# Optimization experiments

Measured on AMD Instinct MI355X. Metric: run time of the kernel, lower is better.

## Reference

```python
import jax, jax.numpy as jnp
import numpy as np
import math

E, N, K, R = 1024, 16, 4, 64  # embed_dim, state_dim, d_conv, dt_rank=ceil(E/16)
B, L = 2, 2048


def setup_inputs() -> dict:
    key = jax.random.key(0)
    ks = jax.random.split(key, 8)
    gn = lambda k, sh, sc: jax.random.normal(k, sh, dtype=jnp.float32) * sc
    W_z = gn(ks[0], (E, E), E ** -0.5)                      # in_proj_z weight (no bias)
    W_params = gn(ks[1], (R + 2 * N, E), E ** -0.5)         # in_proj_params weight (no bias)
    conv_w = gn(ks[2], (E, 1, K), 0.5)                      # depthwise conv1d weight, no bias
    dt_std = R ** -0.5 * 0.1
    W_dt = jax.random.uniform(ks[3], (E, R), jnp.float32, -dt_std, dt_std)
    b_dt = jnp.full((E,), math.log(math.expm1(0.001)), dtype=jnp.float32)
    A_log = jnp.tile(jnp.log(jnp.arange(1, N + 1, dtype=jnp.float32))[None, :], (E, 1))
    D = jnp.ones((E,), dtype=jnp.float32)
    W_out = gn(ks[4], (E, E), E ** -0.5)
    x = jax.random.normal(ks[5], (B, L, E), dtype=jnp.float32)
    return dict(x=x, W_z=W_z, W_params=W_params, conv_w=conv_w, W_dt=W_dt,
                b_dt=b_dt, A_log=A_log, D=D, W_out=W_out)


def reference(x, W_z, W_params, conv_w, W_dt, b_dt, A_log, D, W_out):
    b, l, e = x.shape
    n = A_log.shape[1]
    r = W_dt.shape[1]
    k = conv_w.shape[-1]

    z = x @ W_z.T                                           # [B,L,E]
    params = x @ W_params.T                                 # [B,L,R+2N]
    dt_unproj = params[..., :r]
    # B_proj = params[..., r:r+n] is computed but UNUSED in the original forward
    C_proj = params[..., r + n:]                            # [B,L,N]
    dt = jax.nn.softplus(dt_unproj @ W_dt.T + b_dt)         # [B,L,E]

    # depthwise causal conv: torch pads K-1 both sides then slices [:L] == left-pad K-1
    xc = jax.lax.conv_general_dilated(
        x.transpose(0, 2, 1), conv_w, (1,), [(k - 1, 0)],
        dimension_numbers=('NCH', 'OIH', 'NCH'), feature_group_count=e)
    u = jax.nn.silu(xc.transpose(0, 2, 1))                  # [B,L,E]

    A = -jnp.exp(A_log)                                     # [E,N]
    A_tilde = jnp.exp(dt[..., None] * A[None, None])        # [B,L,E,N]
    B_tilde = jnp.where(jnp.abs(A)[None, None] < 1e-5,
                        dt[..., None],
                        (A_tilde - 1.0) / (A[None, None] + 1e-10))

    # recurrence (note t-1 indexing, faithful to original):
    # h_0 = B~[0]*u[0];  h_t = A~[t-1]*h_{t-1} + B~[t-1]*u[t-1]
    h0 = B_tilde[:, 0] * u[:, 0, :, None]                   # [B,E,N]

    def step(h, inp):
        a, bt, uu = inp
        h_new = a * h + bt * uu[..., None]
        return h_new, h_new

    xs = (A_tilde[:, :-1].transpose(1, 0, 2, 3),
          B_tilde[:, :-1].transpose(1, 0, 2, 3),
          u[:, :-1].transpose(1, 0, 2))
    _, hs = jax.lax.scan(step, h0, xs)                      # [L-1,B,E,N]
    h = jnp.concatenate([h0[None], hs], axis=0).transpose(1, 0, 2, 3)  # [B,L,E,N]

    y = jnp.einsum('bln,blen->ble', C_proj, h)
    y_ssm = y + u * D
    y_gated = y_ssm * jax.nn.silu(z)
    return y_gated @ W_out.T
```

## Files before the change

kernel.cpp:

```cpp
#include <hip/hip_runtime.h>
#include <math.h>

#define B_ 2
#define L_ 2048
#define E_ 1024
#define N_ 16
#define R_ 64
#define PWP 128
#define BL_ (B_*L_)

using bf16x8 = __attribute__((ext_vector_type(8))) short;
using f32x4  = __attribute__((ext_vector_type(4))) float;

__device__ __forceinline__ float softplusf(float x) {
    return fmaxf(x, 0.0f) + log1pf(expf(-fabsf(x)));
}
__device__ __forceinline__ float siluf(float x) {
    return x / (1.0f + expf(-x));
}
__device__ __forceinline__ ushort f2bf(float f) {
    unsigned u = __float_as_uint(f);
    return (ushort)((u + 0x7fffu + ((u >> 16) & 1u)) >> 16);
}
__device__ __forceinline__ float bf2f(ushort h) {
    return __uint_as_float(((unsigned)h) << 16);
}
__device__ __forceinline__ void gload16(const ushort* g, ushort* l) {
    __builtin_amdgcn_global_load_lds((const __attribute__((address_space(1))) void*)g,
                                     (__attribute__((address_space(3))) void*)l, 16, 0, 0);
}

__device__ __forceinline__ void split_body(const float* __restrict__ src, int spitch,
                                           int rows_src, ushort* __restrict__ dst,
                                           int K, int total4, int idx) {
    if (idx >= total4) return;
    const int Kq = K >> 2;
    const int r  = idx / Kq;
    const int c4 = (idx - r * Kq) << 2;
    float f[4] = {0.f, 0.f, 0.f, 0.f};
    if (r < rows_src)
        *reinterpret_cast<float4*>(f) = *reinterpret_cast<const float4*>(src + (size_t)r * spitch + c4);
    ushort h[4], lo[4];
#pragma unroll
    for (int q = 0; q < 4; ++q) {
        h[q]  = f2bf(f[q]);
        lo[q] = f2bf(f[q] - bf2f(h[q]));
    }
    ushort* d0 = dst + (size_t)r * 2 * K + c4;
    *reinterpret_cast<uint2*>(d0)     = make_uint2((uint)h[0]  | ((uint)h[1]  << 16), (uint)h[2]  | ((uint)h[3]  << 16));
    *reinterpret_cast<uint2*>(d0 + K) = make_uint2((uint)lo[0] | ((uint)lo[1] << 16), (uint)lo[2] | ((uint)lo[3] << 16));
}

__global__ __launch_bounds__(256)
void split_rm(const float* __restrict__ src, int spitch, int rows_src,
              ushort* __restrict__ dst, int K, int total4) {
    split_body(src, spitch, rows_src, dst, K, total4, blockIdx.x * 256 + threadIdx.x);
}

__global__ __launch_bounds__(256)
void split_w3(const float* __restrict__ Wz, const float* __restrict__ Wp,
              const float* __restrict__ Wdt, ushort* __restrict__ WzC,
              ushort* __restrict__ WpC, ushort* __restrict__ WdtC) {
    const int idx = blockIdx.x * 256 + threadIdx.x;
    if (blockIdx.y == 0)      split_body(Wz,  E_, E_,  WzC,  E_, E_ * E_ / 4, idx);
    else if (blockIdx.y == 1) split_body(Wp,  E_, 96,  WpC,  E_, 128 * E_ / 4, idx);
    else                      split_body(Wdt, R_, E_,  WdtC, R_, E_ * R_ / 4, idx);
}

__global__ __launch_bounds__(256)
void split_tr(const float* __restrict__ ygT, ushort* __restrict__ Ycat) {
    __shared__ float Ts[64][65];
    const int e0 = blockIdx.x * 64;
    const int l0 = blockIdx.y * 64;
    const int b  = blockIdx.z;
    const int tid = threadIdx.x;
    for (int idx = tid; idx < 64 * 64; idx += 256) {
        const int rr = idx >> 6, cc = idx & 63;
        Ts[rr][cc] = ygT[((size_t)(b * E_ + e0 + rr) << 11) + l0 + cc];
    }
    __syncthreads();
    for (int idx = tid; idx < 64 * 16; idx += 256) {
        const int rl = idx >> 4, g = idx & 15;
        ushort h[4], lo[4];
#pragma unroll
        for (int q = 0; q < 4; ++q) {
            const float f = Ts[g * 4 + q][rl];
            h[q]  = f2bf(f);
            lo[q] = f2bf(f - bf2f(h[q]));
        }
        ushort* d0 = Ycat + (size_t)(b * L_ + l0 + rl) * 2 * E_ + e0 + g * 4;
        *reinterpret_cast<uint2*>(d0)      = make_uint2((uint)h[0]  | ((uint)h[1]  << 16), (uint)h[2]  | ((uint)h[3]  << 16));
        *reinterpret_cast<uint2*>(d0 + E_) = make_uint2((uint)lo[0] | ((uint)lo[1] << 16), (uint)lo[2] | ((uint)lo[3] << 16));
    }
}

template<int BM, int BN, int BK, int MODE>
__global__ __launch_bounds__(256)
void mfma_gemm(const ushort* __restrict__ A, const ushort* __restrict__ Bm,
               const float* __restrict__ bias, ushort* __restrict__ P2,
               float* __restrict__ C2, float* __restrict__ C, int Kd, int Ncols) {
    constexpr int WTM = BM / 2, WTN = BN / 2;
    constexpr int MI = WTM / 16, NJ = WTN / 16;
    constexpr int CPR = BK / 8;
    constexpr int KS  = BK / 32;
    constexpr int RPW = 64 / CPR;
    __shared__ ushort As[BM * BK];
    __shared__ ushort Bs[BN * BK];
    const int tid  = threadIdx.x;
    const int wave = tid >> 6, lane = tid & 63;
    const int m0 = blockIdx.x * BM, n0 = blockIdx.y * BN;
    const int wr = wave >> 1, wc = wave & 1;
    const int fr = lane & 15, fg = lane >> 4;
    const int kxor = (fr & 7) << 3;
    const int pK = 2 * Kd;

    f32x4 acc[MI][NJ];
#pragma unroll
    for (int i = 0; i < MI; ++i)
#pragma unroll
        for (int j = 0; j < NJ; ++j) { f32x4 z = {0.f, 0.f, 0.f, 0.f}; acc[i][j] = z; }

    const int lrow = lane / CPR;
    const int lc   = lane % CPR;

    const int KP = Kd / BK;
    for (int seg = 0; seg < 3; ++seg) {
        const int ao = (seg == 2) ? Kd : 0;
        const int bo = (seg == 1) ? Kd : 0;
        for (int tt = 0; tt < KP; ++tt) {
            const int ka = ao + tt * BK, kb = bo + tt * BK;
#pragma unroll
            for (int g = 0; g < BM / (4 * RPW); ++g) {
                const int srow = (wave * (BM / (4 * RPW)) + g) * RPW + lrow;
                const int sc = (lc & 8) | ((lc ^ (srow & 7)) & 7);
                gload16(A + (size_t)(m0 + srow) * pK + ka + sc * 8, As + srow * BK + lc * 8);
            }
#pragma unroll
            for (int g = 0; g < BN / (4 * RPW); ++g) {
                const int srow = (wave * (BN / (4 * RPW)) + g) * RPW + lrow;
                const int sc = (lc & 8) | ((lc ^ (srow & 7)) & 7);
                gload16(Bm + (size_t)(n0 + srow) * pK + kb + sc * 8, Bs + srow * BK + lc * 8);
            }
            __syncthreads();

#pragma unroll
            for (int ks = 0; ks < KS; ++ks) {
                bf16x8 av[MI], bv[NJ];
#pragma unroll
                for (int i = 0; i < MI; ++i) {
                    const int row = wr * WTM + i * 16 + fr;
                    av[i] = *reinterpret_cast<const bf16x8*>(&As[row * BK + ((ks * 32 + fg * 8) ^ kxor)]);
                }
#pragma unroll
                for (int j = 0; j < NJ; ++j) {
                    const int row = wc * WTN + j * 16 + fr;
                    bv[j] = *reinterpret_cast<const bf16x8*>(&Bs[row * BK + ((ks * 32 + fg * 8) ^ kxor)]);
                }
#pragma unroll
                for (int i = 0; i < MI; ++i)
#pragma unroll
                    for (int j = 0; j < NJ; ++j)
                        acc[i][j] = __builtin_amdgcn_mfma_f32_16x16x32_bf16(av[i], bv[j], acc[i][j], 0, 0, 0);
            }
            __syncthreads();
        }
    }

    if constexpr (MODE == 0) {
#pragma unroll
        for (int i = 0; i < MI; ++i) {
            const int m = m0 + wr * WTM + i * 16 + fg * 4;
#pragma unroll
            for (int j = 0; j < NJ; ++j) {
                const int n = n0 + wc * WTN + j * 16 + fr;
#pragma unroll
                for (int r = 0; r < 4; ++r)
                    C[(size_t)(m + r) * Ncols + n] = acc[i][j][r];
            }
        }
    } else if constexpr (MODE == 2) {
        const int b  = n0 >> 11;
        const int lb = n0 - (b << 11);
#pragma unroll
        for (int i = 0; i < MI; ++i) {
            const int e = m0 + wr * WTM + i * 16 + fg * 4;
#pragma unroll
            for (int r = 0; r < 4; ++r) {
                const float bia = bias[e + r];
                float* row = C + ((size_t)(b * E_ + e + r) << 11) + lb;
#pragma unroll
                for (int j = 0; j < NJ; ++j)
                    row[wc * WTN + j * 16 + fr] = softplusf(acc[i][j][r] + bia);
            }
        }
    } else {
        if (m0 < 1024) {
            const int b  = n0 >> 11;
            const int lb = n0 - (b << 11);
#pragma unroll
            for (int i = 0; i < MI; ++i) {
                const int e = m0 + wr * WTM + i * 16 + fg * 4;
#pragma unroll
                for (int r = 0; r < 4; ++r) {
                    float* row = C + ((size_t)(b * E_ + e + r) << 11) + lb;
#pragma unroll
                    for (int j = 0; j < NJ; ++j)
                        row[wc * WTN + j * 16 + fr] = acc[i][j][r];
                }
            }
        } else {
#pragma unroll
            for (int i = 0; i < MI; ++i) {
                const int cb = m0 - 1024 + wr * WTM + i * 16 + fg * 4;
#pragma unroll
                for (int j = 0; j < NJ; ++j) {
                    const int bl = n0 + wc * WTN + j * 16 + fr;
#pragma unroll
                    for (int r = 0; r < 4; ++r) {
                        const float v = acc[i][j][r];
                        const int cix = cb + r;
                        if (cix < 64) {
                            const ushort hh = f2bf(v);
                            P2[(size_t)bl * 128 + cix]      = hh;
                            P2[(size_t)bl * 128 + 64 + cix] = f2bf(v - bf2f(hh));
                        } else if (cix >= 80 && cix < 96) {
                            C2[(size_t)bl * PWP + cix] = v;
                        }
                    }
                }
            }
        }
    }
}

__global__ __launch_bounds__(256)
void conv_split_kernel(const float* __restrict__ x, const float* __restrict__ cw,
                       float* __restrict__ uT, ushort* __restrict__ Xcat) {
    __shared__ float Xt[67][65];
    const int e0 = blockIdx.x * 64;
    const int l0 = blockIdx.y * 64;
    const int b  = blockIdx.z;
    const int tid = threadIdx.x;
    for (int idx = tid; idx < 67 * 64; idx += 256) {
        const int row = idx >> 6, col = idx & 63;
        const int gl = l0 - 3 + row;
        Xt[row][col] = (gl >= 0) ? x[((size_t)b * L_ + gl) * E_ + e0 + col] : 0.0f;
    }
    __syncthreads();
    const int lL = tid & 63;
    const int w  = tid >> 6;
    for (int ee = w; ee < 64; ee += 4) {
        const int e = e0 + ee;
        const float w0 = cw[e*4+0], w1 = cw[e*4+1], w2 = cw[e*4+2], w3 = cw[e*4+3];
        const float v = w0*Xt[lL][ee] + w1*Xt[lL+1][ee] + w2*Xt[lL+2][ee] + w3*Xt[lL+3][ee];
        uT[((size_t)b * E_ + e) * L_ + l0 + lL] = siluf(v);
    }
    for (int idx = tid; idx < 64 * 16; idx += 256) {
        const int rl = idx >> 4, g = idx & 15;
        ushort h[4], lo[4];
#pragma unroll
        for (int q = 0; q < 4; ++q) {
            const float f = Xt[3 + rl][g * 4 + q];
            h[q]  = f2bf(f);
            lo[q] = f2bf(f - bf2f(h[q]));
        }
        ushort* d0 = Xcat + (size_t)(b * L_ + l0 + rl) * 2 * E_ + e0 + g * 4;
        *reinterpret_cast<uint2*>(d0)      = make_uint2((uint)h[0]  | ((uint)h[1]  << 16), (uint)h[2]  | ((uint)h[3]  << 16));
        *reinterpret_cast<uint2*>(d0 + E_) = make_uint2((uint)lo[0] | ((uint)lo[1] << 16), (uint)lo[2] | ((uint)lo[3] << 16));
    }
}

__global__ __launch_bounds__(64)
void scan_kernel(const float* __restrict__ dtT, const float* __restrict__ uT,
                 const float* __restrict__ zT, const float* __restrict__ params,
                 const float* __restrict__ A_log, const float* __restrict__ Dp,
                 float* __restrict__ ygT) {
    __shared__ float sdt[64 * 33];
    __shared__ float su [64 * 33];
    const int c = blockIdx.x;
    const int b = c >> 10;
    const int e = c & (E_ - 1);
    const int lane = threadIdx.x;
    constexpr int CH = L_ / 64;
    constexpr float LOG2E = 1.44269504088896340736f;

    const float* dtp = dtT + ((size_t)b * E_ + e) * L_;
    const float* up  = uT  + ((size_t)b * E_ + e) * L_;
    const float* zp  = zT  + ((size_t)b * E_ + e) * L_;

#pragma unroll
    for (int it = 0; it < 8; ++it) {
        const int l = (it * 64 + lane) * 4;
        const int slot = ((l >> 5) * 33) + (l & 31);
        float4 vd = *reinterpret_cast<const float4*>(dtp + l);
        float4 vu = *reinterpret_cast<const float4*>(up  + l);
        sdt[slot] = vd.x; sdt[slot+1] = vd.y; sdt[slot+2] = vd.z; sdt[slot+3] = vd.w;
        su [slot] = vu.x; su [slot+1] = vu.y; su [slot+2] = vu.z; su [slot+3] = vu.w;
    }

    float An2[N_], rA[N_];
    unsigned selm = 0;
#pragma unroll
    for (int n = 0; n < N_; ++n) {
        const float A = -expf(A_log[e * N_ + n]);
        An2[n] = A * LOG2E;
        if (fabsf(A) < 1e-5f) selm |= (1u << n);
        rA[n] = 1.0f / (A + 1e-10f);
    }
    const float Dv = Dp[e];
    __syncthreads();

    const int base = lane * 33;
    const float d0 = sdt[0];
    const float u0 = su[0];

    float h[N_];
    float dsum = 0.0f;
#pragma unroll
    for (int n = 0; n < N_; ++n) h[n] = 0.0f;
#pragma unroll 4
    for (int j = 0; j < CH; ++j) {
        const float d  = sdt[base + j];
        const float uu = su [base + j];
        dsum += d;
#pragma unroll
        for (int n = 0; n < N_; ++n) {
            const float at = __builtin_amdgcn_exp2f(d * An2[n]);
            const float bt = ((selm >> n) & 1u) ? d : (at - 1.0f) * rA[n];
            h[n] = fmaf(at, h[n], bt * uu);
        }
    }
    float P[N_];
#pragma unroll
    for (int n = 0; n < N_; ++n) P[n] = __builtin_amdgcn_exp2f(dsum * An2[n]);

#pragma unroll
    for (int off = 1; off < 64; off <<= 1) {
#pragma unroll
        for (int n = 0; n < N_; ++n) {
            const float Pp = __shfl_up(P[n], off);
            const float Lp = __shfl_up(h[n], off);
            if (lane >= off) {
                h[n] = fmaf(P[n], Lp, h[n]);
                P[n] *= Pp;
            }
        }
    }

    float cP[N_], cL[N_];
#pragma unroll
    for (int n = 0; n < N_; ++n) {
        cP[n] = __shfl_up(P[n], 1);
        cL[n] = __shfl_up(h[n], 1);
    }

#pragma unroll
    for (int n = 0; n < N_; ++n) {
        const float at0 = __builtin_amdgcn_exp2f(d0 * An2[n]);
        const float bt0 = ((selm >> n) & 1u) ? d0 : (at0 - 1.0f) * rA[n];
        const float g0 = bt0 * u0;
        h[n] = (lane == 0) ? g0 : fmaf(cP[n], g0, cL[n]);
    }

    const float* crow = params + (size_t)b * L_ * PWP + 80;
    const int l0 = lane * CH;
    float4 pc0, pc1, pc2, pc3;
    {
        const float4* Cp4 = reinterpret_cast<const float4*>(crow + (size_t)l0 * PWP);
        pc0 = Cp4[0]; pc1 = Cp4[1]; pc2 = Cp4[2]; pc3 = Cp4[3];
    }
    float pz = zp[l0];
#pragma unroll 4
    for (int j = 0; j < CH; ++j) {
        float4 nc0, nc1, nc2, nc3; float nz = 0.0f;
        if (j < CH - 1) {
            const float4* Np = reinterpret_cast<const float4*>(crow + (size_t)(l0 + j + 1) * PWP);
            nc0 = Np[0]; nc1 = Np[1]; nc2 = Np[2]; nc3 = Np[3];
            nz = zp[l0 + j + 1];
        }
        const float d  = sdt[base + j];
        const float uu = su [base + j];
        float y = 0.0f;
        y = fmaf(pc0.x, h[0],  y); y = fmaf(pc0.y, h[1],  y);
        y = fmaf(pc0.z, h[2],  y); y = fmaf(pc0.w, h[3],  y);
        y = fmaf(pc1.x, h[4],  y); y = fmaf(pc1.y, h[5],  y);
        y = fmaf(pc1.z, h[6],  y); y = fmaf(pc1.w, h[7],  y);
        y = fmaf(pc2.x, h[8],  y); y = fmaf(pc2.y, h[9],  y);
        y = fmaf(pc2.z, h[10], y); y = fmaf(pc2.w, h[11], y);
        y = fmaf(pc3.x, h[12], y); y = fmaf(pc3.y, h[13], y);
        y = fmaf(pc3.z, h[14], y); y = fmaf(pc3.w, h[15], y);
        const float outv = (y + uu * Dv) * siluf(pz);
        if (j < CH - 1) {
#pragma unroll
            for (int n = 0; n < N_; ++n) {
                const float at = __builtin_amdgcn_exp2f(d * An2[n]);
                const float bt = ((selm >> n) & 1u) ? d : (at - 1.0f) * rA[n];
                h[n] = fmaf(at, h[n], bt * uu);
            }
        }
        sdt[base + j] = outv;
        pc0 = nc0; pc1 = nc1; pc2 = nc2; pc3 = nc3; pz = nz;
    }
    __syncthreads();

    float* yp = ygT + ((size_t)b * E_ + e) * L_;
#pragma unroll
    for (int it = 0; it < 8; ++it) {
        const int l = (it * 64 + lane) * 4;
        const int slot = ((l >> 5) * 33) + (l & 31);
        float4 o;
        o.x = sdt[slot]; o.y = sdt[slot+1]; o.z = sdt[slot+2]; o.w = sdt[slot+3];
        *reinterpret_cast<float4*>(yp + l) = o;
    }
}

extern "C" void kernel_launch(void* const* d_in, const int* in_sizes, int n_in,
                              void* d_out, int out_size, void* d_ws, size_t ws_size,
                              hipStream_t stream) {
    const float* x     = (const float*)d_in[0];
    const float* W_z   = (const float*)d_in[1];
    const float* W_p   = (const float*)d_in[2];
    const float* cw    = (const float*)d_in[3];
    const float* W_dt  = (const float*)d_in[4];
    const float* b_dt  = (const float*)d_in[5];
    const float* A_log = (const float*)d_in[6];
    const float* Dp    = (const float*)d_in[7];
    const float* W_out = (const float*)d_in[8];
    float* out = (float*)d_out;

    char* w = (char*)d_ws;
    ushort* Xcat   = (ushort*)(w);
    ushort* Wzpcat = (ushort*)(w + 16777216);
    ushort* Wpcat  = (ushort*)(w + 20971520);
    ushort* Wdtcat = (ushort*)(w + 21495808);
    ushort* Pcat   = (ushort*)(w + 21757952);
    float*  params = (float*)(w + 22806528);
    float*  zT     = (float*)(w + 24903680);
    float*  dtT    = (float*)(w + 41680896);
    float*  uT     = (float*)(w + 58458112);
    float*  ygT    = (float*)(w + 75235328);
    ushort* Ycat   = Xcat;
    ushort* Wocat  = Wzpcat;

    conv_split_kernel<<<dim3(E_ / 64, L_ / 64, B_), 256, 0, stream>>>(x, cw, uT, Xcat);
    split_w3<<<dim3(1024, 3), 256, 0, stream>>>(W_z, W_p, W_dt, Wzpcat, Wpcat, Wdtcat);
    mfma_gemm<128,64,128,4><<<dim3(1152 / 128, BL_ / 64), 256, 0, stream>>>(
        Wzpcat, Xcat, nullptr, Pcat, params, zT, E_, 0);
    mfma_gemm<128,64,64,2><<<dim3(E_ / 128, BL_ / 64), 256, 0, stream>>>(
        Wdtcat, Pcat, b_dt, nullptr, nullptr, dtT, R_, 0);
    scan_kernel<<<B_ * E_, 64, 0, stream>>>(dtT, uT, zT, params, A_log, Dp, ygT);
    split_tr<<<dim3(E_ / 64, L_ / 64, B_), 256, 0, stream>>>(ygT, Ycat);
    split_rm<<<1024, 256, 0, stream>>>(W_out, E_, E_, Wocat, E_, E_ * E_ / 4);
    mfma_gemm<128,64,128,0><<<dim3(BL_ / 128, E_ / 64), 256, 0, stream>>>(
        Ycat, Wocat, nullptr, nullptr, nullptr, out, E_, E_);
}
```

Baseline: 274.5 us.

## Split selective scan across sequence halves with a pre-pass carry kernel

Adds a pre-pass kernel that computes the decay product and state aggregate of the first half of the sequence for each (batch, channel) and stores them in scratch space that aliases the consumed Xcat buffer. The main scan kernel then launches twice as many blocks, each covering half the sequence with 16-step chunks per lane, and half-1 blocks seed their carry from the stored aggregate. The aim is to double the number of waves and reduce per-wave serial latency, since 2048 single-wave blocks leave CUs underoccupied. The cost is recomputing the first half's scan in an extra launch, plus a dependent kernel boundary.

```diff
diff --git a/kernel.cpp b/kernel.cpp
--- a/kernel.cpp
+++ b/kernel.cpp
@@ -271,25 +271,21 @@
 }
 
 __global__ __launch_bounds__(64)
-void scan_kernel(const float* __restrict__ dtT, const float* __restrict__ uT,
-                 const float* __restrict__ zT, const float* __restrict__ params,
-                 const float* __restrict__ A_log, const float* __restrict__ Dp,
-                 float* __restrict__ ygT) {
-    __shared__ float sdt[64 * 33];
-    __shared__ float su [64 * 33];
+void scan_sum_kernel(const float* __restrict__ dtT, const float* __restrict__ uT,
+                     const float* __restrict__ A_log, float* __restrict__ gsum) {
+    __shared__ float sdt[32 * 33];
+    __shared__ float su [32 * 33];
     const int c = blockIdx.x;
     const int b = c >> 10;
     const int e = c & (E_ - 1);
     const int lane = threadIdx.x;
-    constexpr int CH = L_ / 64;
+    constexpr int CH = 16;
     constexpr float LOG2E = 1.44269504088896340736f;
 
     const float* dtp = dtT + ((size_t)b * E_ + e) * L_;
     const float* up  = uT  + ((size_t)b * E_ + e) * L_;
-    const float* zp  = zT  + ((size_t)b * E_ + e) * L_;
-
-#pragma unroll
-    for (int it = 0; it < 8; ++it) {
+#pragma unroll
+    for (int it = 0; it < 4; ++it) {
         const int l = (it * 64 + lane) * 4;
         const int slot = ((l >> 5) * 33) + (l & 31);
         float4 vd = *reinterpret_cast<const float4*>(dtp + l);
@@ -297,7 +293,6 @@
         sdt[slot] = vd.x; sdt[slot+1] = vd.y; sdt[slot+2] = vd.z; sdt[slot+3] = vd.w;
         su [slot] = vu.x; su [slot+1] = vu.y; su [slot+2] = vu.z; su [slot+3] = vu.w;
     }
-
     float An2[N_], rA[N_];
     unsigned selm = 0;
 #pragma unroll
@@ -307,13 +302,9 @@
         if (fabsf(A) < 1e-5f) selm |= (1u << n);
         rA[n] = 1.0f / (A + 1e-10f);
     }
-    const float Dv = Dp[e];
     __syncthreads();
 
-    const int base = lane * 33;
-    const float d0 = sdt[0];
-    const float u0 = su[0];
-
+    const int base = (lane >> 1) * 33 + (lane & 1) * 16;
     float h[N_];
     float dsum = 0.0f;
 #pragma unroll
@@ -346,7 +337,95 @@
             }
         }
     }
-
+    if (lane == 63) {
+#pragma unroll
+        for (int n = 0; n < N_; ++n) {
+            gsum[(size_t)c * 32 + n]      = P[n];
+            gsum[(size_t)c * 32 + 16 + n] = h[n];
+        }
+    }
+}
+
+__global__ __launch_bounds__(64)
+void scan_kernel(const float* __restrict__ dtT, const float* __restrict__ uT,
+                 const float* __restrict__ zT, const float* __restrict__ params,
+                 const float* __restrict__ A_log, const float* __restrict__ Dp,
+                 const float* __restrict__ gsum, float* __restrict__ ygT) {
+    __shared__ float sdt[32 * 33];
+    __shared__ float su [32 * 33];
+    const int idx = blockIdx.x;
+    const int c = idx >> 1, half = idx & 1;
+    const int b = c >> 10;
+    const int e = c & (E_ - 1);
+    const int lane = threadIdx.x;
+    constexpr int CH = 16;
+    constexpr float LOG2E = 1.44269504088896340736f;
+
+    const float* chdt = dtT + ((size_t)b * E_ + e) * L_;
+    const float* chu  = uT  + ((size_t)b * E_ + e) * L_;
+    const float* dtp = chdt + half * 1024;
+    const float* up  = chu  + half * 1024;
+    const float* zp  = zT + ((size_t)b * E_ + e) * L_ + half * 1024;
+
+    const float d0 = chdt[0];
+    const float u0 = chu[0];
+
+#pragma unroll
+    for (int it = 0; it < 4; ++it) {
+        const int l = (it * 64 + lane) * 4;
+        const int slot = ((l >> 5) * 33) + (l & 31);
+        float4 vd = *reinterpret_cast<const float4*>(dtp + l);
+        float4 vu = *reinterpret_cast<const float4*>(up  + l);
+        sdt[slot] = vd.x; sdt[slot+1] = vd.y; sdt[slot+2] = vd.z; sdt[slot+3] = vd.w;
+        su [slot] = vu.x; su [slot+1] = vu.y; su [slot+2] = vu.z; su [slot+3] = vu.w;
+    }
+
+    float An2[N_], rA[N_];
+    unsigned selm = 0;
+#pragma unroll
+    for (int n = 0; n < N_; ++n) {
+        const float A = -expf(A_log[e * N_ + n]);
+        An2[n] = A * LOG2E;
+        if (fabsf(A) < 1e-5f) selm |= (1u << n);
+        rA[n] = 1.0f / (A + 1e-10f);
+    }
+    const float Dv = Dp[e];
+    __syncthreads();
+
+    const int base = (lane >> 1) * 33 + (lane & 1) * 16;
+
+    float h[N_];
+    float dsum = 0.0f;
+#pragma unroll
+    for (int n = 0; n < N_; ++n) h[n] = 0.0f;
+#pragma unroll 4
+    for (int j = 0; j < CH; ++j) {
+        const float d  = sdt[base + j];
+        const float uu = su [base + j];
+        dsum += d;
+#pragma unroll
+        for (int n = 0; n < N_; ++n) {
+            const float at = __builtin_amdgcn_exp2f(d * An2[n]);
+            const float bt = ((selm >> n) & 1u) ? d : (at - 1.0f) * rA[n];
+            h[n] = fmaf(at, h[n], bt * uu);
+        }
+    }
+    float P[N_];
+#pragma unroll
+    for (int n = 0; n < N_; ++n) P[n] = __builtin_amdgcn_exp2f(dsum * An2[n]);
+
+#pragma unroll
+    for (int off = 1; off < 64; off <<= 1) {
+#pragma unroll
+        for (int n = 0; n < N_; ++n) {
+            const float Pp = __shfl_up(P[n], off);
+            const float Lp = __shfl_up(h[n], off);
+            if (lane >= off) {
+                h[n] = fmaf(P[n], Lp, h[n]);
+                P[n] *= Pp;
+            }
+        }
+    }
     float cP[N_], cL[N_];
 #pragma unroll
     for (int n = 0; n < N_; ++n) {
@@ -356,27 +435,36 @@
 
 #pragma unroll
     for (int n = 0; n < N_; ++n) {
+        const float pl = (lane == 0) ? 1.0f : cP[n];
+        const float ll = (lane == 0) ? 0.0f : cL[n];
+        float fP = pl, fL = ll;
+        if (half == 1) {
+            const float Ph = gsum[(size_t)c * 32 + n];
+            const float Lh = gsum[(size_t)c * 32 + 16 + n];
+            fP = pl * Ph;
+            fL = fmaf(pl, Lh, ll);
+        }
         const float at0 = __builtin_amdgcn_exp2f(d0 * An2[n]);
         const float bt0 = ((selm >> n) & 1u) ? d0 : (at0 - 1.0f) * rA[n];
-        const float g0 = bt0 * u0;
-        h[n] = (lane == 0) ? g0 : fmaf(cP[n], g0, cL[n]);
-    }
-
+        const float g0  = bt0 * u0;
+        h[n] = fmaf(fP, g0, fL);
+    }
+
+    const int l0g = half * 1024 + lane * CH;
     const float* crow = params + (size_t)b * L_ * PWP + 80;
-    const int l0 = lane * CH;
     float4 pc0, pc1, pc2, pc3;
     {
-        const float4* Cp4 = reinterpret_cast<const float4*>(crow + (size_t)l0 * PWP);
+        const float4* Cp4 = reinterpret_cast<const float4*>(crow + (size_t)l0g * PWP);
         pc0 = Cp4[0]; pc1 = Cp4[1]; pc2 = Cp4[2]; pc3 = Cp4[3];
     }
-    float pz = zp[l0];
+    float pz = zp[lane * CH];
 #pragma unroll 4
     for (int j = 0; j < CH; ++j) {
         float4 nc0, nc1, nc2, nc3; float nz = 0.0f;
         if (j < CH - 1) {
-            const float4* Np = reinterpret_cast<const float4*>(crow + (size_t)(l0 + j + 1) * PWP);
+            const float4* Np = reinterpret_cast<const float4*>(crow + (size_t)(l0g + j + 1) * PWP);
             nc0 = Np[0]; nc1 = Np[1]; nc2 = Np[2]; nc3 = Np[3];
-            nz = zp[l0 + j + 1];
+            nz = zp[lane * CH + j + 1];
         }
         const float d  = sdt[base + j];
         const float uu = su [base + j];
@@ -403,9 +491,9 @@
     }
     __syncthreads();
 
-    float* yp = ygT + ((size_t)b * E_ + e) * L_;
-#pragma unroll
-    for (int it = 0; it < 8; ++it) {
+    float* yp = ygT + ((size_t)b * E_ + e) * L_ + half * 1024;
+#pragma unroll
+    for (int it = 0; it < 4; ++it) {
         const int l = (it * 64 + lane) * 4;
         const int slot = ((l >> 5) * 33) + (l & 31);
         float4 o;
@@ -439,6 +527,7 @@
     float*  dtT    = (float*)(w + 41680896);
     float*  uT     = (float*)(w + 58458112);
     float*  ygT    = (float*)(w + 75235328);
+    float*  gsum   = (float*)Xcat;
     ushort* Ycat   = Xcat;
     ushort* Wocat  = Wzpcat;
 
@@ -448,7 +537,8 @@
         Wzpcat, Xcat, nullptr, Pcat, params, zT, E_, 0);
     mfma_gemm<128,64,64,2><<<dim3(E_ / 128, BL_ / 64), 256, 0, stream>>>(
         Wdtcat, Pcat, b_dt, nullptr, nullptr, dtT, R_, 0);
-    scan_kernel<<<B_ * E_, 64, 0, stream>>>(dtT, uT, zT, params, A_log, Dp, ygT);
+    scan_sum_kernel<<<B_ * E_, 64, 0, stream>>>(dtT, uT, A_log, gsum);
+    scan_kernel<<<2 * B_ * E_, 64, 0, stream>>>(dtT, uT, zT, params, A_log, Dp, gsum, ygT);
     split_tr<<<dim3(E_ / 64, L_ / 64, B_), 256, 0, stream>>>(ygT, Ycat);
     split_rm<<<1024, 256, 0, stream>>>(W_out, E_, E_, Wocat, E_, E_ * E_ / 4);
     mfma_gemm<128,64,128,0><<<dim3(BL_ / 128, E_ / 64), 256, 0, stream>>>(
```

Measured after the change: 283.5 us. +3.3%, slower.
